# Optimization experiments

Measured on AMD Instinct MI355X. Metric: run time of the kernel, lower is better.

Reference implementation:

```python
import jax, jax.numpy as jnp
import numpy as np

B, S, H = 2, 1024, 2048
NH, HD = 16, 128
PAST = 1024
ROPE_THETA = 10000.0


def _rope(q, k, theta=ROPE_THETA):
    # q, k: [B, S, NH, HD]; standard rotate-half RoPE over current positions 0..S-1
    s, d = q.shape[1], q.shape[3]
    inv_freq = 1.0 / (theta ** (jnp.arange(0, d, 2, dtype=jnp.float32) / d))  # [d/2]
    freqs = jnp.arange(s, dtype=jnp.float32)[:, None] * inv_freq[None, :]      # [S, d/2]
    emb = jnp.concatenate([freqs, freqs], axis=-1)                             # [S, d]
    cos = jnp.cos(emb)[None, :, None, :]
    sin = jnp.sin(emb)[None, :, None, :]

    def rot_half(x):
        x1, x2 = jnp.split(x, 2, axis=-1)
        return jnp.concatenate([-x2, x1], axis=-1)

    return q * cos + rot_half(q) * sin, k * cos + rot_half(k) * sin


def setup_inputs() -> dict:
    key = jax.random.key(0)
    ks = jax.random.split(key, 12)
    hidden_states = jax.random.normal(ks[0], (B, S, H), dtype=jnp.float32)
    past_key = jax.random.normal(ks[1], (B, NH, PAST, HD), dtype=jnp.float32)
    past_value = jax.random.normal(ks[2], (B, NH, PAST, HD), dtype=jnp.float32)
    # causal mask accounting for cache: 1.0 where masked (query i cannot see kv j > PAST+i)
    q_pos = PAST + jnp.arange(S)[:, None]
    kv_pos = jnp.arange(PAST + S)[None, :]
    mask = jnp.broadcast_to((kv_pos > q_pos).astype(jnp.float32)[None, None], (B, 1, S, PAST + S))
    sc = 1.0 / np.sqrt(H)
    Wq = jax.random.normal(ks[3], (H, NH * HD), dtype=jnp.float32) * sc
    Wk = jax.random.normal(ks[4], (H, NH * HD), dtype=jnp.float32) * sc
    Wv = jax.random.normal(ks[5], (H, NH * HD), dtype=jnp.float32) * sc
    Wo = jax.random.normal(ks[6], (NH * HD, H), dtype=jnp.float32) * (1.0 / np.sqrt(NH * HD))
    bq = jnp.zeros((NH * HD,), jnp.float32)
    bk = jnp.zeros((NH * HD,), jnp.float32)
    bv = jnp.zeros((NH * HD,), jnp.float32)
    bo = jnp.zeros((H,), jnp.float32)
    return {"hidden_states": hidden_states, "mask": mask, "past_key": past_key,
            "past_value": past_value, "Wq": Wq, "bq": bq, "Wk": Wk, "bk": bk,
            "Wv": Wv, "bv": bv, "Wo": Wo, "bo": bo}


def reference(hidden_states, mask, past_key, past_value, Wq, bq, Wk, bk, Wv, bv, Wo, bo):
    b, s, _ = hidden_states.shape
    scale = 1.0 / jnp.sqrt(jnp.float32(HD))
    q = (hidden_states @ Wq + bq).reshape(b, s, NH, HD)
    k = (hidden_states @ Wk + bk).reshape(b, s, NH, HD)
    v = (hidden_states @ Wv + bv).reshape(b, s, NH, HD)
    q, k = _rope(q, k)
    q, k, v = (jnp.transpose(x, (0, 2, 1, 3)) for x in (q, k, v))  # [B,NH,S,HD]
    k = jnp.concatenate([past_key, k], axis=2)    # [B,NH,S_total,HD]
    v = jnp.concatenate([past_value, v], axis=2)
    scores = jnp.einsum('bhqd,bhkd->bhqk', q, k) * scale
    scores = scores + mask * (-1e9)               # mask broadcasts over heads
    probs = jax.nn.softmax(scores, axis=-1).astype(jnp.float32)
    out = jnp.einsum('bhqk,bhkd->bhqd', probs, v)
    out = out.transpose(0, 2, 1, 3).reshape(b, s, NH * HD)
    return out @ Wo + bo, k, v
```

## Files before the change

kernel.cpp:

```cpp
#include <hip/hip_runtime.h>
#include <hip/hip_bf16.h>
#include <math.h>

#define NB 2
#define SEQ 1024
#define HDIM 2048
#define NHEADS 16
#define HDHEAD 128
#define PASTN 1024
#define STOT 2048
#define MROWS 2048

typedef __attribute__((ext_vector_type(4))) float f32x4;
typedef __attribute__((ext_vector_type(8))) __bf16 bf16x8;
typedef __attribute__((ext_vector_type(8))) unsigned short us8;
typedef __attribute__((ext_vector_type(4))) unsigned short us4;

__device__ __forceinline__ unsigned short f2bf(float f) {
    union { float f; unsigned int u; } v; v.f = f;
    unsigned int u = v.u;
    u += 0x7FFFu + ((u >> 16) & 1u);
    return (unsigned short)(u >> 16);
}
__device__ __forceinline__ bf16x8 as_bf(us8 u) { return __builtin_bit_cast(bf16x8, u); }

__device__ __forceinline__ void gl16(const unsigned short* g, unsigned short* l) {
    __builtin_amdgcn_global_load_lds(
        (const __attribute__((address_space(1))) void*)g,
        (__attribute__((address_space(3))) void*)l, 16, 0, 0);
}

#define OFF_CS  ((size_t)0)
#define OFF_HSB (OFF_CS  + (size_t)SEQ*64*8)
#define OFF_WT  (OFF_HSB + (size_t)MROWS*HDIM*2)
#define OFF_QBF (OFF_WT  + (size_t)4*HDIM*HDIM*2)
#define OFF_KC  (OFF_QBF + (size_t)NB*NHEADS*SEQ*HDHEAD*2)
#define OFF_VT  (OFF_KC  + (size_t)NB*NHEADS*STOT*HDHEAD*2)
#define OFF_ATT (OFF_VT  + (size_t)NB*NHEADS*HDHEAD*STOT*2)


__global__ void k_prep1(const float* __restrict__ in, unsigned short* __restrict__ hsb,
                        const float* __restrict__ pk, float* __restrict__ outK,
                        unsigned short* __restrict__ Kc2, float2* __restrict__ csT) {
    const int bid = blockIdx.x, tid = threadIdx.x;
    const int i = (bid * 256 + tid) * 4;
    {
        f32x4 v = *(const f32x4*)(in + i);
        us4 o;
        o.x = f2bf(v.x); o.y = f2bf(v.y); o.z = f2bf(v.z); o.w = f2bf(v.w);
        *(us4*)(hsb + i) = o;
    }
    {
        size_t e = (size_t)i;
        size_t bh = e >> 17;
        int p = (int)((e >> 7) & 1023);
        int d0 = (int)(e & 127);
        f32x4 v = *(const f32x4*)(pk + e);
        __builtin_nontemporal_store(v, (f32x4*)(outK + e + (bh << 17)));
        us4 u;
        u.x = f2bf(v.x); u.y = f2bf(v.y); u.z = f2bf(v.z); u.w = f2bf(v.w);
        const int kt = p >> 6, pr = p & 63;
        *(us4*)(Kc2 + ((bh * 32 + kt) << 13) + (size_t)pr * 128 + (d0 ^ ((p & 7) << 3))) = u;
    }
    if (bid < 256) {
        const int idx = bid * 256 + tid;
        const int s = idx >> 6, fi = idx & 63;
        float inv = 1.0f / powf(10000.0f, (float)fi / 64.0f);
        float a = (float)s * inv;
        csT[idx] = make_float2(cosf(a), sinf(a));
    }
}

__global__ void k_wt(const float* __restrict__ Wq, const float* __restrict__ Wk,
                     const float* __restrict__ Wv, const float* __restrict__ Wo,
                     unsigned short* __restrict__ WT) {
    __shared__ unsigned short t[32][33];
    int z = blockIdx.z;
    const float* W = (z == 0) ? Wq : (z == 1) ? Wk : (z == 2) ? Wv : Wo;
    unsigned short* out = WT + (size_t)z * HDIM * HDIM;
    int n0 = blockIdx.x * 32, k0 = blockIdx.y * 32;
    int tx = threadIdx.x, ty = threadIdx.y;
    #pragma unroll
    for (int j = 0; j < 4; ++j) {
        int kk = ty + j * 8;
        t[kk][tx] = f2bf(W[(size_t)(k0 + kk) * HDIM + n0 + tx]);
    }
    __syncthreads();
    #pragma unroll
    for (int j = 0; j < 4; ++j) {
        int nn = ty + j * 8;
        out[(size_t)(n0 + nn) * HDIM + k0 + tx] = t[tx][nn];
    }
}

__global__ void k_pastv(const float* __restrict__ pv, float* __restrict__ outV,
                        unsigned short* __restrict__ Vt2) {
    __shared__ unsigned short t[64][65];
    int bh = blockIdx.z;
    int p0 = blockIdx.x * 64, d0 = blockIdx.y * 64;
    int tx = threadIdx.x, ty = threadIdx.y;
    const float* src = pv + ((size_t)bh * PASTN + p0) * HDHEAD + d0;
    float* dst = outV + ((size_t)bh * STOT + p0) * HDHEAD + d0;
    #pragma unroll
    for (int j = 0; j < 16; ++j) {
        int pp = ty + j * 4;
        float v = src[(size_t)pp * HDHEAD + tx];
        __builtin_nontemporal_store(v, &dst[(size_t)pp * HDHEAD + tx]);
        t[tx][pp] = f2bf(v);
    }
    __syncthreads();
    unsigned short* vt = Vt2 + (((size_t)bh * 32 + (p0 >> 6)) << 13);
    #pragma unroll
    for (int j = 0; j < 16; ++j) {
        int dd = ty + j * 4;
        const int d = d0 + dd;
        vt[(size_t)d * 64 + (tx ^ ((d & 7) << 3))] = t[dd][tx];
    }
}

__global__ __launch_bounds__(512, 2) void k_gemm_qkv(
    const unsigned short* __restrict__ hsb, const unsigned short* __restrict__ WT,
    const float* __restrict__ bq, const float* __restrict__ bk, const float* __restrict__ bv,
    const float2* __restrict__ csT,
    unsigned short* __restrict__ qbf, unsigned short* __restrict__ Kc2,
    unsigned short* __restrict__ Vt2, float* __restrict__ outK, float* __restrict__ outV) {
    __shared__ __align__(16) unsigned short As[2][256 * 64];
    __shared__ __align__(16) unsigned short Bs[2][256 * 64];

    const int bid = blockIdx.x;
    const int swz = (bid & 7) * 24 + (bid >> 3);
    const int mb = swz & 7;
    const int nbz = swz >> 3;
    const int z = nbz >> 3;
    const int nb8 = nbz & 7;
    const int m0 = mb * 256;
    const int n0 = nb8 * 256;
    const unsigned short* Wz = WT + (size_t)z * HDIM * HDIM;
    const float* bias = (z == 0) ? bq : (z == 1) ? bk : bv;

    const int t = threadIdx.x;
    const int lane = t & 63, wid = t >> 6;
    const int wr = wid >> 1, wc = wid & 1;
    const int c = lane & 15, g = lane >> 4;

    const int lrow8 = lane >> 3;
    const int lslot = (lane & 7) ^ lrow8;
    const unsigned short* aB = hsb + (size_t)(m0 + lrow8) * HDIM + lslot * 8;
    const unsigned short* bB = Wz + (size_t)(n0 + lrow8) * HDIM + lslot * 8;

    auto stage = [&](int kt, int pb) {
        const int k0s = kt * 64;
        #pragma unroll
        for (int j = 0; j < 4; ++j) {
            const int ch = wid * 4 + j;
            gl16(aB + (size_t)(ch * 8) * HDIM + k0s, &As[pb][ch * 512]);
            gl16(bB + (size_t)(ch * 8) * HDIM + k0s, &Bs[pb][ch * 512]);
        }
    };

    f32x4 acc[4][8] = {};
    const int NT = HDIM / 64;

    stage(0, 0);
    stage(1, 1);

    for (int kt = 0; kt < NT; ++kt) {
        const int p = kt & 1;
        if (kt + 1 < NT) {
            asm volatile("s_waitcnt vmcnt(8)" ::: "memory");
        } else {
            asm volatile("s_waitcnt vmcnt(0)" ::: "memory");
        }
        __builtin_amdgcn_s_barrier();
        bf16x8 bfr[8][2];
        #pragma unroll
        for (int ni = 0; ni < 8; ++ni) {
            const int br = wc * 128 + ni * 16 + c;
            const int sw = br & 7;
            bfr[ni][0] = as_bf(*(const us8*)&Bs[p][br * 64 + ((g ^ sw) << 3)]);
            bfr[ni][1] = as_bf(*(const us8*)&Bs[p][br * 64 + (((4 + g) ^ sw) << 3)]);
        }
        #pragma unroll
        for (int mi = 0; mi < 4; ++mi) {
            const int ar = wr * 64 + mi * 16 + c;
            const int swa = ar & 7;
            const bf16x8 a0 = as_bf(*(const us8*)&As[p][ar * 64 + ((g ^ swa) << 3)]);
            const bf16x8 a1 = as_bf(*(const us8*)&As[p][ar * 64 + (((4 + g) ^ swa) << 3)]);
            __builtin_amdgcn_s_setprio(1);
            #pragma unroll
            for (int ni = 0; ni < 8; ++ni)
                acc[mi][ni] = __builtin_amdgcn_mfma_f32_16x16x32_bf16(a0, bfr[ni][0], acc[mi][ni], 0, 0, 0);
            #pragma unroll
            for (int ni = 0; ni < 8; ++ni)
                acc[mi][ni] = __builtin_amdgcn_mfma_f32_16x16x32_bf16(a1, bfr[ni][1], acc[mi][ni], 0, 0, 0);
            __builtin_amdgcn_s_setprio(0);
            __builtin_amdgcn_s_barrier();
        }
        if (kt + 2 < NT) stage(kt + 2, p);
    }

    const float qscale = 0.08838834764831845f * 1.44269504088896f;
    const int h = nb8 * 2 + wc;
    #pragma unroll
    for (int mi = 0; mi < 4; ++mi) {
        #pragma unroll
        for (int r = 0; r < 4; ++r) {
            const int row = m0 + wr * 64 + mi * 16 + g * 4 + r;
            const int b = row >> 10, s = row & 1023;
            const size_t bh2 = (size_t)(b * NHEADS + h);
            const int p = PASTN + s;
            #pragma unroll
            for (int ni = 0; ni < 8; ++ni) {
                const int d = ni * 16 + c;
                const int nglob = n0 + wc * 128 + d;
                const float val = acc[mi][ni][r] + bias[nglob];
                if (z == 2) {
                    __builtin_nontemporal_store(val, &outV[(bh2 * STOT + p) * HDHEAD + d]);
                    Vt2[((bh2 * 32 + (p >> 6)) << 13) + (size_t)d * 64 +
                        ((p & 63) ^ ((d & 7) << 3))] = f2bf(val);
                } else {
                    const int fidx = d & 63;
                    const float2 cs = csT[s * 64 + fidx];
                    const float other = acc[mi][ni ^ 4][r] + bias[nglob ^ 64];
                    const float rot = (d < 64) ? (val * cs.x - other * cs.y)
                                               : (val * cs.x + other * cs.y);
                    if (z == 0) {
                        qbf[(bh2 * SEQ + s) * HDHEAD + d] = f2bf(rot * qscale);
                    } else {
                        Kc2[((bh2 * 32 + (p >> 6)) << 13) + (size_t)(p & 63) * 128 +
                            (d ^ ((p & 7) << 3))] = f2bf(rot);
                        __builtin_nontemporal_store(rot, &outK[(bh2 * STOT + p) * HDHEAD + d]);
                    }
                }
            }
        }
    }
}

__global__ __launch_bounds__(512) void k_attn(
    const unsigned short* __restrict__ qbf, const unsigned short* __restrict__ Kc2,
    const unsigned short* __restrict__ Vt2, unsigned short* __restrict__ attn) {
    __shared__ __align__(16) unsigned short Ks[2][64 * 128];
    __shared__ __align__(16) unsigned short Vs[128 * 64];
    __shared__ __align__(16) unsigned short P[8][16][72];
    const int qt = blockIdx.x;
    const int bh = blockIdx.y;
    const int b = bh >> 4, h = bh & 15;
    const int t = threadIdx.x, lane = t & 63, w = t >> 6;
    const int c = lane & 15, g = lane >> 4;
    const int q0 = qt * 128 + w * 16;
    const unsigned short* Qb = qbf + ((size_t)bh * SEQ + q0) * HDHEAD;
    const unsigned short* Kbase = Kc2 + ((size_t)bh << 18);
    const unsigned short* Vbase = Vt2 + ((size_t)bh << 18);

    bf16x8 qf[4];
    #pragma unroll
    for (int kf = 0; kf < 4; ++kf)
        qf[kf] = as_bf(*(const us8*)(Qb + (size_t)c * HDHEAD + kf * 32 + g * 8));

    #pragma unroll
    for (int j = 0; j < 2; ++j) {
        const int ch = w * 2 + j;
        gl16(Kbase + ch * 512 + lane * 8, &Ks[0][ch * 512]);
    }

    f32x4 o[8] = {};
    float mrow[4] = {-1e30f, -1e30f, -1e30f, -1e30f};
    float lrow[4] = {0.f, 0.f, 0.f, 0.f};
    const int nkt = 18 + 2 * qt;
    int cur = 0;
    for (int kt = 0; kt < nkt; ++kt) {
        asm volatile("s_waitcnt vmcnt(0)" ::: "memory");
        __builtin_amdgcn_s_barrier();
        const unsigned short* Vg = Vbase + ((size_t)kt << 13);
        #pragma unroll
        for (int j = 0; j < 2; ++j) {
            const int ch = w * 2 + j;
            gl16(Vg + ch * 512 + lane * 8, &Vs[ch * 512]);
        }
        if (kt + 1 < nkt) {
            const unsigned short* Kg = Kbase + ((size_t)(kt + 1) << 13);
            #pragma unroll
            for (int j = 0; j < 2; ++j) {
                const int ch = w * 2 + j;
                gl16(Kg + ch * 512 + lane * 8, &Ks[cur ^ 1][ch * 512]);
            }
        }
        f32x4 sa[4] = {};
        #pragma unroll
        for (int nf = 0; nf < 4; ++nf) {
            const int row = nf * 16 + c;
            const int swzr = (row & 7) << 3;
            #pragma unroll
            for (int kf = 0; kf < 4; ++kf) {
                bf16x8 kf8 = as_bf(*(const us8*)&Ks[cur][row * 128 + ((kf * 32 + g * 8) ^ swzr)]);
                sa[nf] = __builtin_amdgcn_mfma_f32_16x16x32_bf16(qf[kf], kf8, sa[nf], 0, 0, 0);
            }
        }
        const int k0 = kt * 64;
        if (k0 + 63 > PASTN + q0) {
            #pragma unroll
            for (int nf = 0; nf < 4; ++nf) {
                const int j = k0 + nf * 16 + c;
                #pragma unroll
                for (int r = 0; r < 4; ++r)
                    if (j > PASTN + q0 + g * 4 + r) sa[nf][r] = -1e30f;
            }
        }
        float pmax[4];
        #pragma unroll
        for (int r = 0; r < 4; ++r)
            pmax[r] = fmaxf(fmaxf(sa[0][r], sa[1][r]), fmaxf(sa[2][r], sa[3][r]));
        bool need = false;
        #pragma unroll
        for (int r = 0; r < 4; ++r) need = need || (pmax[r] > mrow[r] + 12.0f);
        if (__any(need)) {
            #pragma unroll
            for (int r = 0; r < 4; ++r) {
                float mx = pmax[r];
                mx = fmaxf(mx, __shfl_xor(mx, 1));
                mx = fmaxf(mx, __shfl_xor(mx, 2));
                mx = fmaxf(mx, __shfl_xor(mx, 4));
                mx = fmaxf(mx, __shfl_xor(mx, 8));
                const float mnew = fmaxf(mrow[r], mx);
                const float alpha = exp2f(mrow[r] - mnew);
                mrow[r] = mnew;
                lrow[r] *= alpha;
                #pragma unroll
                for (int nd = 0; nd < 8; ++nd) o[nd][r] *= alpha;
            }
        }
        #pragma unroll
        for (int r = 0; r < 4; ++r) {
            const float p0 = exp2f(sa[0][r] - mrow[r]);
            const float p1 = exp2f(sa[1][r] - mrow[r]);
            const float p2 = exp2f(sa[2][r] - mrow[r]);
            const float p3 = exp2f(sa[3][r] - mrow[r]);
            lrow[r] += (p0 + p1) + (p2 + p3);
            P[w][g * 4 + r][0 * 16 + c] = f2bf(p0);
            P[w][g * 4 + r][1 * 16 + c] = f2bf(p1);
            P[w][g * 4 + r][2 * 16 + c] = f2bf(p2);
            P[w][g * 4 + r][3 * 16 + c] = f2bf(p3);
        }
        if (kt + 1 < nkt) {
            asm volatile("s_waitcnt vmcnt(2)" ::: "memory");
        } else {
            asm volatile("s_waitcnt vmcnt(0)" ::: "memory");
        }
        __builtin_amdgcn_s_barrier();
        #pragma unroll
        for (int kf2 = 0; kf2 < 2; ++kf2) {
            const bf16x8 pa = as_bf(*(const us8*)&P[w][c][kf2 * 32 + g * 8]);
            #pragma unroll
            for (int nd = 0; nd < 8; ++nd) {
                const int d = nd * 16 + c;
                const bf16x8 vf = as_bf(*(const us8*)&Vs[d * 64 + ((kf2 * 32 + g * 8) ^ ((d & 7) << 3))]);
                o[nd] = __builtin_amdgcn_mfma_f32_16x16x32_bf16(pa, vf, o[nd], 0, 0, 0);
            }
        }
        cur ^= 1;
    }
    #pragma unroll
    for (int r = 0; r < 4; ++r) {
        float ls = lrow[r];
        ls += __shfl_xor(ls, 1);
        ls += __shfl_xor(ls, 2);
        ls += __shfl_xor(ls, 4);
        ls += __shfl_xor(ls, 8);
        const float inv = 1.0f / ls;
        #pragma unroll
        for (int nd = 0; nd < 8; ++nd) o[nd][r] *= inv;
    }
    #pragma unroll
    for (int nd = 0; nd < 8; ++nd)
        #pragma unroll
        for (int r = 0; r < 4; ++r) {
            const int srow = q0 + g * 4 + r;
            attn[((size_t)b * SEQ + srow) * HDIM + h * HDHEAD + nd * 16 + c] = f2bf(o[nd][r]);
        }
}

__global__ __launch_bounds__(256) void k_gemm_out(
    const unsigned short* __restrict__ attn, const unsigned short* __restrict__ WTo,
    const float* __restrict__ bo, float* __restrict__ out) {
    __shared__ __align__(16) unsigned short As[2][128 * 64];
    __shared__ __align__(16) unsigned short Bs[2][128 * 64];
    const int m0 = blockIdx.y * 128;
    const int n0 = blockIdx.x * 128;
    const int t = threadIdx.x;
    const int lane = t & 63, w = t >> 6;
    const int c = lane & 15, g = lane >> 4;

    const int lrow = lane >> 3;
    const int lslot = (lane & 7) ^ lrow;
    const unsigned short* aB = attn + (size_t)(m0 + lrow) * HDIM + lslot * 8;
    const unsigned short* bB = WTo + (size_t)(n0 + lrow) * HDIM + lslot * 8;

    f32x4 acc[2][8] = {};
    const int NT = HDIM / 64;

    #pragma unroll
    for (int j = 0; j < 4; ++j) {
        const int ch = w * 4 + j;
        gl16(aB + (size_t)(ch * 8) * HDIM, &As[0][ch * 512]);
        gl16(bB + (size_t)(ch * 8) * HDIM, &Bs[0][ch * 512]);
    }
    for (int kt = 0; kt < NT; ++kt) {
        const int cb = kt & 1;
        if (kt + 1 < NT) {
            const int k1 = (kt + 1) * 64;
            #pragma unroll
            for (int j = 0; j < 4; ++j) {
                const int ch = w * 4 + j;
                gl16(aB + (size_t)(ch * 8) * HDIM + k1, &As[cb ^ 1][ch * 512]);
                gl16(bB + (size_t)(ch * 8) * HDIM + k1, &Bs[cb ^ 1][ch * 512]);
            }
            asm volatile("s_waitcnt vmcnt(8)" ::: "memory");
        } else {
            asm volatile("s_waitcnt vmcnt(0)" ::: "memory");
        }
        __builtin_amdgcn_s_barrier();
        #pragma unroll
        for (int kc = 0; kc < 2; ++kc) {
            bf16x8 af[2];
            #pragma unroll
            for (int mi = 0; mi < 2; ++mi) {
                const int ar = w * 32 + mi * 16 + c;
                af[mi] = as_bf(*(const us8*)&As[cb][ar * 64 + (((kc * 4 + g) ^ (ar & 7)) << 3)]);
            }
            #pragma unroll
            for (int ni = 0; ni < 8; ++ni) {
                const int br = ni * 16 + c;
                bf16x8 bfrag = as_bf(*(const us8*)&Bs[cb][br * 64 + (((kc * 4 + g) ^ (br & 7)) << 3)]);
                acc[0][ni] = __builtin_amdgcn_mfma_f32_16x16x32_bf16(af[0], bfrag, acc[0][ni], 0, 0, 0);
                acc[1][ni] = __builtin_amdgcn_mfma_f32_16x16x32_bf16(af[1], bfrag, acc[1][ni], 0, 0, 0);
            }
        }
        __builtin_amdgcn_s_barrier();
    }
    #pragma unroll
    for (int mi = 0; mi < 2; ++mi)
        #pragma unroll
        for (int r = 0; r < 4; ++r) {
            const int row = m0 + w * 32 + mi * 16 + g * 4 + r;
            #pragma unroll
            for (int ni = 0; ni < 8; ++ni) {
                const int f = n0 + ni * 16 + c;
                __builtin_nontemporal_store(acc[mi][ni][r] + bo[f], &out[(size_t)row * HDIM + f]);
            }
        }
}

extern "C" void kernel_launch(void* const* d_in, const int* in_sizes, int n_in,
                              void* d_out, int out_size, void* d_ws, size_t ws_size,
                              hipStream_t stream) {
    const float* hidden = (const float*)d_in[0];
    const float* past_key = (const float*)d_in[2];
    const float* past_value = (const float*)d_in[3];
    const float* Wq = (const float*)d_in[4];
    const float* bq = (const float*)d_in[5];
    const float* Wk = (const float*)d_in[6];
    const float* bk = (const float*)d_in[7];
    const float* Wv = (const float*)d_in[8];
    const float* bv = (const float*)d_in[9];
    const float* Wo = (const float*)d_in[10];
    const float* bo = (const float*)d_in[11];

    float* out0 = (float*)d_out;
    float* outK = out0 + (size_t)NB * SEQ * HDIM;
    float* outV = outK + (size_t)NB * NHEADS * STOT * HDHEAD;

    char* ws = (char*)d_ws;
    float2* csT = (float2*)(ws + OFF_CS);
    unsigned short* hsb = (unsigned short*)(ws + OFF_HSB);
    unsigned short* WT = (unsigned short*)(ws + OFF_WT);
    unsigned short* qbf = (unsigned short*)(ws + OFF_QBF);
    unsigned short* Kc2 = (unsigned short*)(ws + OFF_KC);
    unsigned short* Vt2 = (unsigned short*)(ws + OFF_VT);
    unsigned short* attnb = (unsigned short*)(ws + OFF_ATT);

    k_prep1<<<dim3(4096), dim3(256), 0, stream>>>(hidden, hsb, past_key, outK, Kc2, csT);
    k_wt<<<dim3(64, 64, 4), dim3(32, 8), 0, stream>>>(Wq, Wk, Wv, Wo, WT);
    k_pastv<<<dim3(16, 2, 32), dim3(64, 4), 0, stream>>>(past_value, outV, Vt2);
    k_gemm_qkv<<<dim3(192), dim3(512), 0, stream>>>(
        hsb, WT, bq, bk, bv, csT, qbf, Kc2, Vt2, outK, outV);
    k_attn<<<dim3(8, 32), dim3(512), 0, stream>>>(qbf, Kc2, Vt2, attnb);
    k_gemm_out<<<dim3(16, 16), dim3(256), 0, stream>>>(
        attnb, WT + (size_t)3 * HDIM * HDIM, bo, out0);
}
```

Measured before the change: 239.7 us.

## Merge prep kernels into one launch, stage output GEMM stores via LDS

Folds the three preprocessing kernels (hidden/past-K conversion, weight transpose, past-V transpose) into a single launch that dispatches on block index, and enlarges the weight-transpose tile to 64x64. Nontemporal stores are replaced with ordinary stores for the K/V cache outputs. The output GEMM epilogue now stages accumulators through shared memory so each lane writes contiguous float4 rows with the bias added. The intent is to cut launch overhead and tail gaps and to coalesce output writes, at the cost of extra LDS traffic and barriers in the epilogue.

```diff
diff --git a/kernel.cpp b/kernel.cpp
--- a/kernel.cpp
+++ b/kernel.cpp
@@ -39,82 +39,85 @@
 #define OFF_ATT (OFF_VT  + (size_t)NB*NHEADS*HDHEAD*STOT*2)
 
 
-__global__ void k_prep1(const float* __restrict__ in, unsigned short* __restrict__ hsb,
-                        const float* __restrict__ pk, float* __restrict__ outK,
-                        unsigned short* __restrict__ Kc2, float2* __restrict__ csT) {
+__global__ void k_prep(const float* __restrict__ in, unsigned short* __restrict__ hsb,
+                       const float* __restrict__ pk, float* __restrict__ outK,
+                       unsigned short* __restrict__ Kc2, float2* __restrict__ csT,
+                       const float* __restrict__ Wq, const float* __restrict__ Wk,
+                       const float* __restrict__ Wv, const float* __restrict__ Wo,
+                       unsigned short* __restrict__ WT,
+                       const float* __restrict__ pv, float* __restrict__ outV,
+                       unsigned short* __restrict__ Vt2) {
+    __shared__ unsigned short tsh[64][65];
     const int bid = blockIdx.x, tid = threadIdx.x;
-    const int i = (bid * 256 + tid) * 4;
-    {
-        f32x4 v = *(const f32x4*)(in + i);
-        us4 o;
-        o.x = f2bf(v.x); o.y = f2bf(v.y); o.z = f2bf(v.z); o.w = f2bf(v.w);
-        *(us4*)(hsb + i) = o;
-    }
-    {
-        size_t e = (size_t)i;
-        size_t bh = e >> 17;
-        int p = (int)((e >> 7) & 1023);
-        int d0 = (int)(e & 127);
-        f32x4 v = *(const f32x4*)(pk + e);
-        __builtin_nontemporal_store(v, (f32x4*)(outK + e + (bh << 17)));
-        us4 u;
-        u.x = f2bf(v.x); u.y = f2bf(v.y); u.z = f2bf(v.z); u.w = f2bf(v.w);
-        const int kt = p >> 6, pr = p & 63;
-        *(us4*)(Kc2 + ((bh * 32 + kt) << 13) + (size_t)pr * 128 + (d0 ^ ((p & 7) << 3))) = u;
-    }
-    if (bid < 256) {
-        const int idx = bid * 256 + tid;
-        const int s = idx >> 6, fi = idx & 63;
-        float inv = 1.0f / powf(10000.0f, (float)fi / 64.0f);
-        float a = (float)s * inv;
-        csT[idx] = make_float2(cosf(a), sinf(a));
-    }
-}
-
-__global__ void k_wt(const float* __restrict__ Wq, const float* __restrict__ Wk,
-                     const float* __restrict__ Wv, const float* __restrict__ Wo,
-                     unsigned short* __restrict__ WT) {
-    __shared__ unsigned short t[32][33];
-    int z = blockIdx.z;
-    const float* W = (z == 0) ? Wq : (z == 1) ? Wk : (z == 2) ? Wv : Wo;
-    unsigned short* out = WT + (size_t)z * HDIM * HDIM;
-    int n0 = blockIdx.x * 32, k0 = blockIdx.y * 32;
-    int tx = threadIdx.x, ty = threadIdx.y;
-    #pragma unroll
-    for (int j = 0; j < 4; ++j) {
-        int kk = ty + j * 8;
-        t[kk][tx] = f2bf(W[(size_t)(k0 + kk) * HDIM + n0 + tx]);
-    }
-    __syncthreads();
-    #pragma unroll
-    for (int j = 0; j < 4; ++j) {
-        int nn = ty + j * 8;
-        out[(size_t)(n0 + nn) * HDIM + k0 + tx] = t[tx][nn];
-    }
-}
-
-__global__ void k_pastv(const float* __restrict__ pv, float* __restrict__ outV,
-                        unsigned short* __restrict__ Vt2) {
-    __shared__ unsigned short t[64][65];
-    int bh = blockIdx.z;
-    int p0 = blockIdx.x * 64, d0 = blockIdx.y * 64;
-    int tx = threadIdx.x, ty = threadIdx.y;
-    const float* src = pv + ((size_t)bh * PASTN + p0) * HDHEAD + d0;
-    float* dst = outV + ((size_t)bh * STOT + p0) * HDHEAD + d0;
-    #pragma unroll
-    for (int j = 0; j < 16; ++j) {
-        int pp = ty + j * 4;
-        float v = src[(size_t)pp * HDHEAD + tx];
-        __builtin_nontemporal_store(v, &dst[(size_t)pp * HDHEAD + tx]);
-        t[tx][pp] = f2bf(v);
-    }
-    __syncthreads();
-    unsigned short* vt = Vt2 + (((size_t)bh * 32 + (p0 >> 6)) << 13);
-    #pragma unroll
-    for (int j = 0; j < 16; ++j) {
-        int dd = ty + j * 4;
-        const int d = d0 + dd;
-        vt[(size_t)d * 64 + (tx ^ ((d & 7) << 3))] = t[dd][tx];
+    if (bid < 4096) {
+        const int i = (bid * 256 + tid) * 4;
+        {
+            f32x4 v = *(const f32x4*)(in + i);
+            us4 o;
+            o.x = f2bf(v.x); o.y = f2bf(v.y); o.z = f2bf(v.z); o.w = f2bf(v.w);
+            *(us4*)(hsb + i) = o;
+        }
+        {
+            size_t e = (size_t)i;
+            size_t bh = e >> 17;
+            int p = (int)((e >> 7) & 1023);
+            int d0 = (int)(e & 127);
+            f32x4 v = *(const f32x4*)(pk + e);
+            *(f32x4*)(outK + e + (bh << 17)) = v;
+            us4 u;
+            u.x = f2bf(v.x); u.y = f2bf(v.y); u.z = f2bf(v.z); u.w = f2bf(v.w);
+            const int kt = p >> 6, pr = p & 63;
+            *(us4*)(Kc2 + ((bh * 32 + kt) << 13) + (size_t)pr * 128 + (d0 ^ ((p & 7) << 3))) = u;
+        }
+        if (bid < 256) {
+            const int idx = bid * 256 + tid;
+            const int s = idx >> 6, fi = idx & 63;
+            float inv = 1.0f / powf(10000.0f, (float)fi / 64.0f);
+            float a = (float)s * inv;
+            csT[idx] = make_float2(cosf(a), sinf(a));
+        }
+    } else if (bid < 8192) {
+        const int idx = bid - 4096;
+        const int z = idx >> 10;
+        const int rem = idx & 1023;
+        const int n0 = (rem & 31) * 64, k0 = (rem >> 5) * 64;
+        const float* W = (z == 0) ? Wq : (z == 1) ? Wk : (z == 2) ? Wv : Wo;
+        unsigned short* out = WT + (size_t)z * HDIM * HDIM;
+        const int tx = tid & 63, ty = tid >> 6;
+        #pragma unroll
+        for (int j = 0; j < 16; ++j) {
+            const int kk = ty + j * 4;
+            tsh[tx][kk] = f2bf(W[(size_t)(k0 + kk) * HDIM + n0 + tx]);
+        }
+        __syncthreads();
+        #pragma unroll
+        for (int j = 0; j < 16; ++j) {
+            const int nn = ty + j * 4;
+            out[(size_t)(n0 + nn) * HDIM + k0 + tx] = tsh[nn][tx];
+        }
+    } else {
+        const int idx = bid - 8192;
+        const int bh = idx >> 5;
+        const int rem = idx & 31;
+        const int p0 = (rem & 15) * 64, d0 = (rem >> 4) * 64;
+        const int tx = tid & 63, ty = tid >> 6;
+        const float* src = pv + ((size_t)bh * PASTN + p0) * HDHEAD + d0;
+        float* dst = outV + ((size_t)bh * STOT + p0) * HDHEAD + d0;
+        #pragma unroll
+        for (int j = 0; j < 16; ++j) {
+            const int pp = ty + j * 4;
+            float v = src[(size_t)pp * HDHEAD + tx];
+            dst[(size_t)pp * HDHEAD + tx] = v;
+            tsh[tx][pp] = f2bf(v);
+        }
+        __syncthreads();
+        unsigned short* vt = Vt2 + (((size_t)bh * 32 + (p0 >> 6)) << 13);
+        #pragma unroll
+        for (int j = 0; j < 16; ++j) {
+            const int dd = ty + j * 4;
+            const int d = d0 + dd;
+            vt[(size_t)d * 64 + (tx ^ ((d & 7) << 3))] = tsh[dd][tx];
+        }
     }
 }
 
@@ -215,7 +218,7 @@
                 const int nglob = n0 + wc * 128 + d;
                 const float val = acc[mi][ni][r] + bias[nglob];
                 if (z == 2) {
-                    __builtin_nontemporal_store(val, &outV[(bh2 * STOT + p) * HDHEAD + d]);
+                    outV[(bh2 * STOT + p) * HDHEAD + d] = val;
                     Vt2[((bh2 * 32 + (p >> 6)) << 13) + (size_t)d * 64 +
                         ((p & 63) ^ ((d & 7) << 3))] = f2bf(val);
                 } else {
@@ -229,7 +232,7 @@
                     } else {
                         Kc2[((bh2 * 32 + (p >> 6)) << 13) + (size_t)(p & 63) * 128 +
                             (d ^ ((p & 7) << 3))] = f2bf(rot);
-                        __builtin_nontemporal_store(rot, &outK[(bh2 * STOT + p) * HDHEAD + d]);
+                        outK[(bh2 * STOT + p) * HDHEAD + d] = rot;
                     }
                 }
             }
@@ -383,8 +386,9 @@
 __global__ __launch_bounds__(256) void k_gemm_out(
     const unsigned short* __restrict__ attn, const unsigned short* __restrict__ WTo,
     const float* __restrict__ bo, float* __restrict__ out) {
-    __shared__ __align__(16) unsigned short As[2][128 * 64];
-    __shared__ __align__(16) unsigned short Bs[2][128 * 64];
+    __shared__ __align__(16) unsigned char SMEM[65536];
+    unsigned short* As0 = (unsigned short*)SMEM;
+    unsigned short* Bs0 = (unsigned short*)(SMEM + 32768);
     const int m0 = blockIdx.y * 128;
     const int n0 = blockIdx.x * 128;
     const int t = threadIdx.x;
@@ -402,8 +406,8 @@
     #pragma unroll
     for (int j = 0; j < 4; ++j) {
         const int ch = w * 4 + j;
-        gl16(aB + (size_t)(ch * 8) * HDIM, &As[0][ch * 512]);
-        gl16(bB + (size_t)(ch * 8) * HDIM, &Bs[0][ch * 512]);
+        gl16(aB + (size_t)(ch * 8) * HDIM, &As0[ch * 512]);
+        gl16(bB + (size_t)(ch * 8) * HDIM, &Bs0[ch * 512]);
     }
     for (int kt = 0; kt < NT; ++kt) {
         const int cb = kt & 1;
@@ -412,8 +416,8 @@
             #pragma unroll
             for (int j = 0; j < 4; ++j) {
                 const int ch = w * 4 + j;
-                gl16(aB + (size_t)(ch * 8) * HDIM + k1, &As[cb ^ 1][ch * 512]);
-                gl16(bB + (size_t)(ch * 8) * HDIM + k1, &Bs[cb ^ 1][ch * 512]);
+                gl16(aB + (size_t)(ch * 8) * HDIM + k1, &As0[(cb ^ 1) * 8192 + ch * 512]);
+                gl16(bB + (size_t)(ch * 8) * HDIM + k1, &Bs0[(cb ^ 1) * 8192 + ch * 512]);
             }
             asm volatile("s_waitcnt vmcnt(8)" ::: "memory");
         } else {
@@ -426,29 +430,41 @@
             #pragma unroll
             for (int mi = 0; mi < 2; ++mi) {
                 const int ar = w * 32 + mi * 16 + c;
-                af[mi] = as_bf(*(const us8*)&As[cb][ar * 64 + (((kc * 4 + g) ^ (ar & 7)) << 3)]);
+                af[mi] = as_bf(*(const us8*)&As0[cb * 8192 + ar * 64 + (((kc * 4 + g) ^ (ar & 7)) << 3)]);
             }
             #pragma unroll
             for (int ni = 0; ni < 8; ++ni) {
                 const int br = ni * 16 + c;
-                bf16x8 bfrag = as_bf(*(const us8*)&Bs[cb][br * 64 + (((kc * 4 + g) ^ (br & 7)) << 3)]);
+                bf16x8 bfrag = as_bf(*(const us8*)&Bs0[cb * 8192 + br * 64 + (((kc * 4 + g) ^ (br & 7)) << 3)]);
                 acc[0][ni] = __builtin_amdgcn_mfma_f32_16x16x32_bf16(af[0], bfrag, acc[0][ni], 0, 0, 0);
                 acc[1][ni] = __builtin_amdgcn_mfma_f32_16x16x32_bf16(af[1], bfrag, acc[1][ni], 0, 0, 0);
             }
         }
         __builtin_amdgcn_s_barrier();
     }
-    #pragma unroll
-    for (int mi = 0; mi < 2; ++mi)
+
+    float* myF = (float*)SMEM + w * (16 * 132);
+    const int qrow = lane & 31;
+    for (int mi = 0; mi < 2; ++mi) {
+        __syncthreads();
         #pragma unroll
         for (int r = 0; r < 4; ++r) {
-            const int row = m0 + w * 32 + mi * 16 + g * 4 + r;
-            #pragma unroll
-            for (int ni = 0; ni < 8; ++ni) {
-                const int f = n0 + ni * 16 + c;
-                __builtin_nontemporal_store(acc[mi][ni][r] + bo[f], &out[(size_t)row * HDIM + f]);
-            }
-        }
+            const int row = g * 4 + r;
+            #pragma unroll
+            for (int ni = 0; ni < 8; ++ni)
+                myF[row * 132 + ni * 16 + c] = acc[mi][ni][r];
+        }
+        __syncthreads();
+        #pragma unroll
+        for (int j = 0; j < 8; ++j) {
+            const int rrow = 2 * j + (lane >> 5);
+            const int row = m0 + w * 32 + mi * 16 + rrow;
+            f32x4 v4 = *(const f32x4*)&myF[rrow * 132 + qrow * 4];
+            const f32x4 b4 = *(const f32x4*)&bo[n0 + qrow * 4];
+            v4 += b4;
+            *(f32x4*)&out[(size_t)row * HDIM + n0 + qrow * 4] = v4;
+        }
+    }
 }
 
 extern "C" void kernel_launch(void* const* d_in, const int* in_sizes, int n_in,
@@ -479,9 +495,9 @@
     unsigned short* Vt2 = (unsigned short*)(ws + OFF_VT);
     unsigned short* attnb = (unsigned short*)(ws + OFF_ATT);
 
-    k_prep1<<<dim3(4096), dim3(256), 0, stream>>>(hidden, hsb, past_key, outK, Kc2, csT);
-    k_wt<<<dim3(64, 64, 4), dim3(32, 8), 0, stream>>>(Wq, Wk, Wv, Wo, WT);
-    k_pastv<<<dim3(16, 2, 32), dim3(64, 4), 0, stream>>>(past_value, outV, Vt2);
+    k_prep<<<dim3(9216), dim3(256), 0, stream>>>(
+        hidden, hsb, past_key, outK, Kc2, csT,
+        Wq, Wk, Wv, Wo, WT, past_value, outV, Vt2);
     k_gemm_qkv<<<dim3(192), dim3(512), 0, stream>>>(
         hsb, WT, bq, bk, bv, csT, qbf, Kc2, Vt2, outK, outV);
     k_attn<<<dim3(8, 32), dim3(512), 0, stream>>>(qbf, Kc2, Vt2, attnb);
```

New measurement: 234.3 us. 2.2% less time.
